# Optimization experiments

Measured on AMD Instinct MI355X. Metric: run time of the kernel, lower is better.

Reference implementation:

```python
import jax, jax.numpy as jnp
import numpy as np

BS, NQ, DIMS = 4, 6400, 256
NH, NL, NP, NQUEUE = 8, 1, 4, 2


def ms_deform_attn(value, shapes_np, starts_np, loc, attn):
    # value: [B, Nv, H, D]; loc: [B, Nq, H, L, P, 2] in [0,1]; attn: [B, Nq, H, L, P]
    B, Nv, H, D = value.shape
    _, Nq, _, L, P, _ = loc.shape
    out = jnp.zeros((B, H, Nq, D), loc.dtype)
    for l in range(L):
        Hl, Wl = int(shapes_np[l, 0]), int(shapes_np[l, 1])
        s = int(starts_np[l])
        vl = value[:, s:s + Hl * Wl].transpose(0, 2, 1, 3)  # [B,H,HW,D]
        # grid_sample align_corners=False pixel coords
        x = loc[:, :, :, l, :, 0] * Wl - 0.5  # [B,Nq,H,P]
        y = loc[:, :, :, l, :, 1] * Hl - 0.5
        x0 = jnp.floor(x); y0 = jnp.floor(y)
        dx = x - x0; dy = y - y0
        x0i = x0.astype(jnp.int32); y0i = y0.astype(jnp.int32)
        acc = jnp.zeros((B, H, Nq * P, D), loc.dtype)
        corners = [(x0i, y0i, (1 - dx) * (1 - dy)),
                   (x0i + 1, y0i, dx * (1 - dy)),
                   (x0i, y0i + 1, (1 - dx) * dy),
                   (x0i + 1, y0i + 1, dx * dy)]
        for xi, yi, w in corners:
            valid = (xi >= 0) & (xi < Wl) & (yi >= 0) & (yi < Hl)
            idx = jnp.clip(yi, 0, Hl - 1) * Wl + jnp.clip(xi, 0, Wl - 1)  # [B,Nq,H,P]
            idx_t = idx.transpose(0, 2, 1, 3).reshape(B, H, Nq * P, 1)
            g = jnp.take_along_axis(vl, idx_t, axis=2)  # [B,H,Nq*P,D]
            wv = jnp.where(valid, w, 0.0).transpose(0, 2, 1, 3).reshape(B, H, Nq * P, 1)
            acc = acc + g * wv
        acc = acc.reshape(B, H, Nq, P, D)
        wl = attn[:, :, :, l].transpose(0, 2, 1, 3)  # [B,H,Nq,P]
        out = out + jnp.einsum('bhnpd,bhnp->bhnd', acc, wl)
    return out.transpose(0, 2, 1, 3).reshape(B, Nq, H * D)


def setup_inputs() -> dict:
    key = jax.random.key(0)
    ks = jax.random.split(key, 12)
    d2 = DIMS * NQUEUE
    noff = NQUEUE * NH * NL * NP * 2
    nattn = NQUEUE * NH * NL * NP
    sc = 1.0 / np.sqrt(DIMS)
    return {
        'query': jax.random.normal(ks[0], (BS, NQ, DIMS), jnp.float32),
        'voxbev': jax.random.normal(ks[1], (BS, NQ, DIMS), jnp.float32),
        'reference_points': jax.random.uniform(ks[2], (BS * NQUEUE, NQ, NL, 2), jnp.float32),
        'spatial_shapes': jnp.array([[80, 80]], dtype=jnp.int64),
        'level_start_index': jnp.array([0], dtype=jnp.int64),
        'Wv': jax.random.normal(ks[3], (DIMS, DIMS), jnp.float32) * sc,
        'bv': jax.random.normal(ks[4], (DIMS,), jnp.float32) * 0.01,
        'Woff': jax.random.normal(ks[5], (d2, noff), jnp.float32) * (1.0 / np.sqrt(d2)),
        'boff': jax.random.normal(ks[6], (noff,), jnp.float32),
        'Wattn': jax.random.normal(ks[7], (d2, nattn), jnp.float32) * (1.0 / np.sqrt(d2)),
        'battn': jax.random.normal(ks[8], (nattn,), jnp.float32) * 0.01,
        'Wo': jax.random.normal(ks[9], (DIMS, DIMS), jnp.float32) * sc,
        'bo': jax.random.normal(ks[10], (DIMS,), jnp.float32) * 0.01,
    }


def reference(query, voxbev, reference_points, spatial_shapes, level_start_index,
              Wv, bv, Woff, boff, Wattn, battn, Wo, bo):
    bs, nq, dims = query.shape
    shapes_np = np.asarray(spatial_shapes)
    starts_np = np.asarray(level_start_index)
    identity = query
    # value = stack([query, voxbev], 1).reshape(bs*2, nq, dims) -> interleaved [q0,v0,q1,v1,...]
    value = jnp.stack([query, voxbev], 1).reshape(bs * NQUEUE, nq, dims)
    qcat = jnp.concatenate([value[:bs], query], -1)  # [bs, nq, 2*dims]
    v = (value @ Wv + bv).reshape(bs * NQUEUE, nq, NH, dims // NH)
    off = (qcat @ Woff + boff).reshape(bs, nq, NH, NQUEUE, NL, NP, 2)
    attn = (qcat @ Wattn + battn).reshape(bs, nq, NH, NQUEUE, NL * NP)
    attn = jax.nn.softmax(attn, axis=-1).reshape(bs, nq, NH, NQUEUE, NL, NP)
    attn = attn.transpose(0, 3, 1, 2, 4, 5).reshape(bs * NQUEUE, nq, NH, NL, NP)
    off = off.transpose(0, 3, 1, 2, 4, 5, 6).reshape(bs * NQUEUE, nq, NH, NL, NP, 2)
    # offset normalizer: (W, H) per level
    norm = jnp.stack([spatial_shapes[:, 1], spatial_shapes[:, 0]], -1).astype(off.dtype)  # [L,2]
    loc = reference_points[:, :, None, :, None, :] + off / norm[None, None, None, :, None, :]
    out = ms_deform_attn(v, shapes_np, starts_np, loc, attn)  # [bs*2, nq, dims]
    out = out.reshape(bs, NQUEUE, nq, dims).mean(1)  # mean over queue
    out = out @ Wo + bo
    return out + identity  # dropout is identity in eval
```

## Files before the change

### kernel.cpp

```cpp
#include <hip/hip_runtime.h>
#include <hip/hip_bf16.h>

#define BS   4
#define NQ   6400
#define DIMS 256
#define NH   8
#define NP   4
#define GW   80
#define GH   80

typedef __hip_bfloat16 bf16;
typedef unsigned short ushort;
typedef __attribute__((ext_vector_type(8))) short short8;
typedef __attribute__((ext_vector_type(4))) float floatx4;

union bfu { bf16 h; ushort s; };
__device__ __forceinline__ ushort f2bs(float x) { bfu u; u.h = __float2bfloat16(x); return u.s; }
__device__ __forceinline__ float bs2f(ushort s) { return __uint_as_float(((unsigned)s) << 16); }
__device__ __forceinline__ float ldin(const void* p, size_t i, int isf) {
    return isf ? ((const float*)p)[i] : bs2f(((const ushort*)p)[i]);
}

__global__ void detect_k(const ushort* __restrict__ q, int* flag) {
    __shared__ int s;
    if (threadIdx.x == 0) s = 0;
    __syncthreads();
    int bad = 0;
    for (int j = 0; j < 16; ++j) {
        ushort v = q[threadIdx.x * 16 + j];
        int e = (v >> 7) & 0xFF;
        if (e > 160) bad = 1;
    }
    if (bad) atomicOr(&s, 1);
    __syncthreads();
    if (threadIdx.x == 0) *flag = s;
}

__global__ void wprep_k(
    const void* __restrict__ Wv, const void* __restrict__ bv,
    const void* __restrict__ Woff, const void* __restrict__ boff,
    const void* __restrict__ Wattn, const void* __restrict__ battn,
    const void* __restrict__ Wo, const void* __restrict__ bo,
    const int* __restrict__ flagp,
    ushort* __restrict__ WvT, ushort* __restrict__ WoaT, ushort* __restrict__ WoT,
    float* __restrict__ biasv, float* __restrict__ biasoa, float* __restrict__ biaso)
{
    const int isf = *flagp;
    const int i = blockIdx.x * 256 + threadIdx.x;
    const int n1 = 256 * 256, n2 = n1 + 192 * 512, n3 = n2 + 256 * 256;
    const int n4 = n3 + 256, n5 = n4 + 192, n6 = n5 + 256;
    if (i < n1) {
        int n = i >> 8, k = i & 255;
        WvT[i] = f2bs(ldin(Wv, (size_t)k * 256 + n, isf));
    } else if (i < n2) {
        int j = i - n1, n = j >> 9, k = j & 511;
        float v = (n < 128) ? ldin(Woff, (size_t)k * 128 + n, isf)
                            : ldin(Wattn, (size_t)k * 64 + (n - 128), isf);
        WoaT[j] = f2bs(v);
    } else if (i < n3) {
        int j = i - n2, n = j >> 8, k = j & 255;
        WoT[j] = f2bs(ldin(Wo, (size_t)k * 256 + n, isf));
    } else if (i < n4) {
        biasv[i - n3] = ldin(bv, i - n3, isf);
    } else if (i < n5) {
        int j = i - n4;
        biasoa[j] = (j < 128) ? ldin(boff, j, isf) : ldin(battn, j - 128, isf);
    } else if (i < n6) {
        biaso[i - n5] = ldin(bo, i - n5, isf);
    }
}

__global__ __launch_bounds__(256) void cvt_k(
    const void* __restrict__ query, const void* __restrict__ voxbev,
    const int* __restrict__ flagp,
    uint4* __restrict__ qb, uint4* __restrict__ vbv)
{
    if (*flagp == 0) return;
    const int t = blockIdx.x * 256 + threadIdx.x;
    const int half = 819200;
    const void* src = (t < half) ? query : voxbev;
    uint4* dst = (t < half) ? qb : vbv;
    const int j = (t < half) ? t : t - half;
    const float4* s = (const float4*)src + (size_t)j * 2;
    float4 a = s[0], b = s[1];
    uint4 o;
    o.x = ((unsigned)f2bs(a.y) << 16) | f2bs(a.x);
    o.y = ((unsigned)f2bs(a.w) << 16) | f2bs(a.z);
    o.z = ((unsigned)f2bs(b.y) << 16) | f2bs(b.x);
    o.w = ((unsigned)f2bs(b.w) << 16) | f2bs(b.z);
    dst[j] = o;
}

enum { A_VAL = 0, A_QCAT = 1, A_PLAIN = 2 };
enum { O_BF16 = 0, O_FINAL = 1, O_VPERM = 2, O_OAPERM = 3 };

template <int AMODE, int OMODE, int KTOT, int NX, int MG>
__global__ __launch_bounds__(256) void pgemm_k(
    const ushort* __restrict__ Apl, const ushort* __restrict__ BT,
    const float* __restrict__ biasf, void* __restrict__ C,
    const void* __restrict__ query_raw, const void* __restrict__ voxbev_raw,
    const ushort* __restrict__ qb, const ushort* __restrict__ vbv,
    const int* __restrict__ flagp)
{
    constexpr int N = NX * 64;
    constexpr int NPH = KTOT / 256;
    constexpr int SROW = 264;
    constexpr int CST = 67;
    constexpr int SMEMB = (64 * SROW * 2 > 128 * CST * 4) ? 64 * SROW * 2
                                                          : 128 * CST * 4;
    __shared__ __align__(16) char smem[SMEMB];
    short* pan = (short*)smem;
    float* cbf = (float*)smem;

    const int F = blockIdx.x;
    const int xcd = F & 7, l = F >> 3;
    const int n = l % NX;
    const int mg = (l / NX) * 8 + xcd;
    if (mg >= MG) return;
    const int bm = mg * 256, bn = n * 64;

    const int isf = *flagp;
    const int tid = threadIdx.x;
    const int lane = tid & 63, wv = tid >> 6;
    const int wm = wv * 64;
    const int fr = lane & 15, fq = (lane >> 4) * 8;

    const ushort* qsrc = isf ? qb  : (const ushort*)query_raw;
    const ushort* vsrc = isf ? vbv : (const ushort*)voxbev_raw;
    const ushort* aph[NPH];
    if (AMODE == A_PLAIN) {
        aph[0] = Apl + (size_t)bm * DIMS;
    } else {
        const int b = bm / NQ, q0 = bm - (bm / NQ) * NQ;
        aph[0] = ((b & 1) ? vsrc : qsrc) + (size_t)((b >> 1) * NQ + q0) * DIMS;
        if (AMODE == A_QCAT) aph[1] = qsrc + (size_t)(b * NQ + q0) * DIMS;
    }

    floatx4 acc[4][4] = {};

    for (int ph = 0; ph < NPH; ++ph) {
        if (ph > 0) __syncthreads();
        #pragma unroll
        for (int i = 0; i < 8; ++i) {
            const int c = tid * 8 + i;
            const int row = c >> 5, j = (c & 31) * 8;
            *(uint4*)&pan[row * SROW + j] =
                *(const uint4*)&BT[(size_t)(bn + row) * KTOT + ph * 256 + j];
        }
        __syncthreads();

        const ushort* ab = aph[ph];
        #pragma unroll
        for (int k0 = 0; k0 < 256; k0 += 32) {
            short8 af[4], bf[4];
            #pragma unroll
            for (int mt = 0; mt < 4; ++mt)
                af[mt] = *(const short8*)&ab[(size_t)(wm + mt * 16 + fr) * DIMS + k0 + fq];
            #pragma unroll
            for (int nt = 0; nt < 4; ++nt)
                bf[nt] = *(const short8*)&pan[(nt * 16 + fr) * SROW + k0 + fq];
            #pragma unroll
            for (int mt = 0; mt < 4; ++mt)
                #pragma unroll
                for (int nt = 0; nt < 4; ++nt)
                    acc[mt][nt] = __builtin_amdgcn_mfma_f32_16x16x32_bf16(
                        af[mt], bf[nt], acc[mt][nt], 0, 0, 0);
        }
    }

    const int col = lane & 15, rq = (lane >> 4) * 4;
    const int lbase = wm & 127;
    #pragma unroll
    for (int half = 0; half < 2; ++half) {
        __syncthreads();
        if ((wv >> 1) == half) {
            #pragma unroll
            for (int mt = 0; mt < 4; ++mt)
                #pragma unroll
                for (int nt = 0; nt < 4; ++nt)
                    #pragma unroll
                    for (int r = 0; r < 4; ++r)
                        cbf[(lbase + mt * 16 + rq + r) * CST + nt * 16 + col] =
                            acc[mt][nt][r];
        }
        __syncthreads();

        if (OMODE == O_FINAL && isf) {
            const int r16 = tid >> 4, cc = tid & 15;
            #pragma unroll
            for (int it = 0; it < 8; ++it) {
                const int lr = it * 16 + r16;
                const size_t g = (size_t)(bm + half * 128 + lr);
                float4 x = *(const float4*)&cbf[lr * CST + cc * 4];
                const ushort* rs = qsrc + g * DIMS + bn + cc * 4;
                x.x += biasf[bn + cc * 4 + 0] + bs2f(rs[0]);
                x.y += biasf[bn + cc * 4 + 1] + bs2f(rs[1]);
                x.z += biasf[bn + cc * 4 + 2] + bs2f(rs[2]);
                x.w += biasf[bn + cc * 4 + 3] + bs2f(rs[3]);
                *(float4*)((float*)C + g * N + bn + cc * 4) = x;
            }
        } else {
            const int r8 = tid >> 3, c8 = tid & 7;
            #pragma unroll
            for (int it = 0; it < 4; ++it) {
                const int lr = it * 32 + r8;
                const size_t g = (size_t)(bm + half * 128 + lr);
                float4 x0 = *(const float4*)&cbf[lr * CST + c8 * 8];
                float4 x1 = *(const float4*)&cbf[lr * CST + c8 * 8 + 4];
                float xs[8] = { x0.x, x0.y, x0.z, x0.w, x1.x, x1.y, x1.z, x1.w };
                #pragma unroll
                for (int e = 0; e < 8; ++e) xs[e] += biasf[bn + c8 * 8 + e];
                if (OMODE == O_FINAL) {
                    const ushort* rs = qsrc + g * DIMS + bn + c8 * 8;
                    #pragma unroll
                    for (int e = 0; e < 8; ++e) xs[e] += bs2f(rs[e]);
                }
                uint4 o;
                o.x = ((unsigned)f2bs(xs[1]) << 16) | f2bs(xs[0]);
                o.y = ((unsigned)f2bs(xs[3]) << 16) | f2bs(xs[2]);
                o.z = ((unsigned)f2bs(xs[5]) << 16) | f2bs(xs[4]);
                o.w = ((unsigned)f2bs(xs[7]) << 16) | f2bs(xs[6]);
                ushort* dstp;
                if (OMODE == O_VPERM) {
                    const int cc = bn + c8 * 8;
                    const int s = (int)(g / NQ), qq = (int)(g % NQ);
                    dstp = (ushort*)C + ((size_t)(s * 8 + (cc >> 5)) * NQ + qq) * 32
                                      + (cc & 31);
                } else if (OMODE == O_OAPERM) {
                    const int cc = bn + c8 * 8;
                    const int bb = (int)(g / NQ), qq = (int)(g % NQ);
                    int hh, off;
                    if (cc < 128) { hh = cc >> 4; off = cc & 15; }
                    else          { hh = (cc - 128) >> 3; off = 16; }
                    dstp = (ushort*)C + ((size_t)(bb * 8 + hh) * NQ + qq) * 24 + off;
                } else {
                    dstp = (ushort*)C + g * N + bn + c8 * 8;
                }
                *(uint4*)dstp = o;
            }
        }
    }
}

__global__ __launch_bounds__(256) void sample_k(
    const ushort* __restrict__ v,
    const ushort* __restrict__ offp,
    const void* __restrict__ refpts,
    const int* __restrict__ flagp,
    ushort* __restrict__ sampled)
{
    const int isf = *flagp;
    __shared__ int   sidx[64][2][17];
    __shared__ float swt [64][2][17];
    const int tid = threadIdx.x;
    const int j = blockIdx.x;
    const int h = j & 7;
    const int k = j >> 3;
    const int b = k / 100;
    const int q0 = (k % 100) * 64;

    if (tid < 128) {
        const int lq = tid >> 1, queue = tid & 1;
        const int q = q0 + lq;
        const ushort* rec = offp + ((size_t)(b * 8 + h) * NQ + q) * 24;
        const ushort* al = rec + 16 + queue * 4;
        float l0 = bs2f(al[0]), l1 = bs2f(al[1]), l2 = bs2f(al[2]), l3 = bs2f(al[3]);
        float mx = fmaxf(fmaxf(l0, l1), fmaxf(l2, l3));
        float e0 = __expf(l0 - mx), e1 = __expf(l1 - mx);
        float e2 = __expf(l2 - mx), e3 = __expf(l3 - mx);
        float inv = 0.5f / (e0 + e1 + e2 + e3);
        const int bq = b * 2 + queue;
        const float rx = ldin(refpts, ((size_t)bq * NQ + q) * 2 + 0, isf);
        const float ry = ldin(refpts, ((size_t)bq * NQ + q) * 2 + 1, isf);
        const ushort* od = rec + queue * 8;
        float ww[4] = { e0 * inv, e1 * inv, e2 * inv, e3 * inv };
        #pragma unroll
        for (int p = 0; p < NP; ++p) {
            const float x = rx * (float)GW + bs2f(od[p * 2 + 0]) - 0.5f;
            const float y = ry * (float)GH + bs2f(od[p * 2 + 1]) - 0.5f;
            const float x0f = floorf(x), y0f = floorf(y);
            const float dx = x - x0f, dy = y - y0f;
            const int x0 = (int)x0f, y0 = (int)y0f;
            const float wp = ww[p];
            const float cw4[4] = { wp * (1.0f - dx) * (1.0f - dy),
                                   wp * dx * (1.0f - dy),
                                   wp * (1.0f - dx) * dy,
                                   wp * dx * dy };
            #pragma unroll
            for (int c = 0; c < 4; ++c) {
                const int xs = x0 + (c & 1), ys = y0 + (c >> 1);
                const bool ok = (unsigned)xs < (unsigned)GW && (unsigned)ys < (unsigned)GH;
                const int xi = min(max(xs, 0), GW - 1);
                const int yi = min(max(ys, 0), GH - 1);
                sidx[lq][queue][p * 4 + c] = yi * GW + xi;
                swt [lq][queue][p * 4 + c] = ok ? cw4[c] : 0.0f;
            }
        }
    }
    __syncthreads();

    const int lq = tid >> 2, d8 = tid & 3;
    const int q = q0 + lq;
    float a[8] = {};
    #pragma unroll
    for (int queue = 0; queue < 2; ++queue) {
        const ushort* vb = v + (((size_t)(b * 2 + queue) * 8 + h) * NQ) * 32 + d8 * 8;
        #pragma unroll
        for (int hf = 0; hf < 2; ++hf) {
            uint4 g[8];
            #pragma unroll
            for (int u = 0; u < 8; ++u) {
                const int ci = sidx[lq][queue][hf * 8 + u];
                g[u] = *(const uint4*)&vb[(size_t)ci * 32];
            }
            __builtin_amdgcn_sched_barrier(0);
            #pragma unroll
            for (int u = 0; u < 8; ++u) {
                const float cw = swt[lq][queue][hf * 8 + u];
                a[0] += cw * bs2f((ushort)g[u].x); a[1] += cw * bs2f((ushort)(g[u].x >> 16));
                a[2] += cw * bs2f((ushort)g[u].y); a[3] += cw * bs2f((ushort)(g[u].y >> 16));
                a[4] += cw * bs2f((ushort)g[u].z); a[5] += cw * bs2f((ushort)(g[u].z >> 16));
                a[6] += cw * bs2f((ushort)g[u].w); a[7] += cw * bs2f((ushort)(g[u].w >> 16));
            }
        }
    }
    uint4 o;
    o.x = ((unsigned)f2bs(a[1]) << 16) | f2bs(a[0]);
    o.y = ((unsigned)f2bs(a[3]) << 16) | f2bs(a[2]);
    o.z = ((unsigned)f2bs(a[5]) << 16) | f2bs(a[4]);
    o.w = ((unsigned)f2bs(a[7]) << 16) | f2bs(a[6]);
    *(uint4*)&sampled[((size_t)b * NQ + q) * DIMS + h * 32 + d8 * 8] = o;
}

extern "C" void kernel_launch(void* const* d_in, const int* in_sizes, int n_in,
                              void* d_out, int out_size, void* d_ws, size_t ws_size,
                              hipStream_t stream)
{
    const void* query  = d_in[0];
    const void* voxbev = d_in[1];
    const void* refpts = d_in[2];
    const void* Wv   = d_in[5];  const void* bv    = d_in[6];
    const void* Woff = d_in[7];  const void* boff  = d_in[8];
    const void* Wattn= d_in[9];  const void* battn = d_in[10];
    const void* Wo   = d_in[11]; const void* bo    = d_in[12];

    char* p = (char*)d_ws;
    int* flag = (int*)p;             p += 256;
    ushort* WvT  = (ushort*)p;       p += 256 * 256 * 2;
    ushort* WoaT = (ushort*)p;       p += 192 * 512 * 2;
    ushort* WoT  = (ushort*)p;       p += 256 * 256 * 2;
    float* biasv  = (float*)p;       p += 1024;
    float* biasoa = (float*)p;       p += 1024;
    float* biaso  = (float*)p;       p += 1024;
    ushort* qb   = (ushort*)p;       p += (size_t)BS * NQ * DIMS * 2;
    ushort* vbv  = (ushort*)p;       p += (size_t)BS * NQ * DIMS * 2;
    ushort* v_ws = (ushort*)p;       p += (size_t)2 * BS * NQ * DIMS * 2;
    ushort* offraw = (ushort*)p;     p += (size_t)BS * NQ * 192 * 2;
    ushort* sampled = (ushort*)p;

    detect_k<<<1, 256, 0, stream>>>((const ushort*)query, flag);
    wprep_k<<<899, 256, 0, stream>>>(Wv, bv, Woff, boff, Wattn, battn, Wo, bo,
                                     flag, WvT, WoaT, WoT, biasv, biasoa, biaso);
    cvt_k<<<6400, 256, 0, stream>>>(query, voxbev, flag, (uint4*)qb, (uint4*)vbv);

    pgemm_k<A_VAL, O_VPERM, 256, 4, 200><<<800, 256, 0, stream>>>(
        nullptr, WvT, biasv, (void*)v_ws, query, voxbev, qb, vbv, flag);

    pgemm_k<A_QCAT, O_OAPERM, 512, 3, 100><<<312, 256, 0, stream>>>(
        nullptr, WoaT, biasoa, (void*)offraw, query, voxbev, qb, vbv, flag);

    sample_k<<<3200, 256, 0, stream>>>(v_ws, offraw, refpts, flag, sampled);

    pgemm_k<A_PLAIN, O_FINAL, 256, 4, 100><<<416, 256, 0, stream>>>(
        sampled, WoT, biaso, d_out, query, voxbev, qb, vbv, flag);
}
```

Before: 217.6 us.

## Merge prep kernels, stage offsets in LDS, and software-pipeline sampling gathers

```diff
diff --git a/kernel.cpp b/kernel.cpp
--- a/kernel.cpp
+++ b/kernel.cpp
@@ -36,59 +36,58 @@
     if (threadIdx.x == 0) *flag = s;
 }
 
-__global__ void wprep_k(
+__global__ __launch_bounds__(256) void prep_k(
     const void* __restrict__ Wv, const void* __restrict__ bv,
     const void* __restrict__ Woff, const void* __restrict__ boff,
     const void* __restrict__ Wattn, const void* __restrict__ battn,
     const void* __restrict__ Wo, const void* __restrict__ bo,
     const int* __restrict__ flagp,
     ushort* __restrict__ WvT, ushort* __restrict__ WoaT, ushort* __restrict__ WoT,
-    float* __restrict__ biasv, float* __restrict__ biasoa, float* __restrict__ biaso)
+    float* __restrict__ biasv, float* __restrict__ biasoa, float* __restrict__ biaso,
+    const void* __restrict__ query, const void* __restrict__ voxbev,
+    uint4* __restrict__ qb, uint4* __restrict__ vbv)
 {
     const int isf = *flagp;
-    const int i = blockIdx.x * 256 + threadIdx.x;
-    const int n1 = 256 * 256, n2 = n1 + 192 * 512, n3 = n2 + 256 * 256;
-    const int n4 = n3 + 256, n5 = n4 + 192, n6 = n5 + 256;
-    if (i < n1) {
-        int n = i >> 8, k = i & 255;
-        WvT[i] = f2bs(ldin(Wv, (size_t)k * 256 + n, isf));
-    } else if (i < n2) {
-        int j = i - n1, n = j >> 9, k = j & 511;
-        float v = (n < 128) ? ldin(Woff, (size_t)k * 128 + n, isf)
-                            : ldin(Wattn, (size_t)k * 64 + (n - 128), isf);
-        WoaT[j] = f2bs(v);
-    } else if (i < n3) {
-        int j = i - n2, n = j >> 8, k = j & 255;
-        WoT[j] = f2bs(ldin(Wo, (size_t)k * 256 + n, isf));
-    } else if (i < n4) {
-        biasv[i - n3] = ldin(bv, i - n3, isf);
-    } else if (i < n5) {
-        int j = i - n4;
-        biasoa[j] = (j < 128) ? ldin(boff, j, isf) : ldin(battn, j - 128, isf);
-    } else if (i < n6) {
-        biaso[i - n5] = ldin(bo, i - n5, isf);
-    }
-}
-
-__global__ __launch_bounds__(256) void cvt_k(
-    const void* __restrict__ query, const void* __restrict__ voxbev,
-    const int* __restrict__ flagp,
-    uint4* __restrict__ qb, uint4* __restrict__ vbv)
-{
-    if (*flagp == 0) return;
-    const int t = blockIdx.x * 256 + threadIdx.x;
-    const int half = 819200;
-    const void* src = (t < half) ? query : voxbev;
-    uint4* dst = (t < half) ? qb : vbv;
-    const int j = (t < half) ? t : t - half;
-    const float4* s = (const float4*)src + (size_t)j * 2;
-    float4 a = s[0], b = s[1];
-    uint4 o;
-    o.x = ((unsigned)f2bs(a.y) << 16) | f2bs(a.x);
-    o.y = ((unsigned)f2bs(a.w) << 16) | f2bs(a.z);
-    o.z = ((unsigned)f2bs(b.y) << 16) | f2bs(b.x);
-    o.w = ((unsigned)f2bs(b.w) << 16) | f2bs(b.z);
-    dst[j] = o;
+    const int bid = blockIdx.x;
+    if (bid < 899) {
+        const int i = bid * 256 + threadIdx.x;
+        const int n1 = 256 * 256, n2 = n1 + 192 * 512, n3 = n2 + 256 * 256;
+        const int n4 = n3 + 256, n5 = n4 + 192, n6 = n5 + 256;
+        if (i < n1) {
+            int n = i >> 8, k = i & 255;
+            WvT[i] = f2bs(ldin(Wv, (size_t)k * 256 + n, isf));
+        } else if (i < n2) {
+            int j = i - n1, n = j >> 9, k = j & 511;
+            float v = (n < 128) ? ldin(Woff, (size_t)k * 128 + n, isf)
+                                : ldin(Wattn, (size_t)k * 64 + (n - 128), isf);
+            WoaT[j] = f2bs(v);
+        } else if (i < n3) {
+            int j = i - n2, n = j >> 8, k = j & 255;
+            WoT[j] = f2bs(ldin(Wo, (size_t)k * 256 + n, isf));
+        } else if (i < n4) {
+            biasv[i - n3] = ldin(bv, i - n3, isf);
+        } else if (i < n5) {
+            int j = i - n4;
+            biasoa[j] = (j < 128) ? ldin(boff, j, isf) : ldin(battn, j - 128, isf);
+        } else if (i < n6) {
+            biaso[i - n5] = ldin(bo, i - n5, isf);
+        }
+    } else {
+        if (isf == 0) return;
+        const int t = (bid - 899) * 256 + threadIdx.x;
+        const int half = 819200;
+        const void* src = (t < half) ? query : voxbev;
+        uint4* dst = (t < half) ? qb : vbv;
+        const int j = (t < half) ? t : t - half;
+        const float4* s = (const float4*)src + (size_t)j * 2;
+        float4 a = s[0], b = s[1];
+        uint4 o;
+        o.x = ((unsigned)f2bs(a.y) << 16) | f2bs(a.x);
+        o.y = ((unsigned)f2bs(a.w) << 16) | f2bs(a.z);
+        o.z = ((unsigned)f2bs(b.y) << 16) | f2bs(b.x);
+        o.w = ((unsigned)f2bs(b.w) << 16) | f2bs(b.z);
+        dst[j] = o;
+    }
 }
 
 enum { A_VAL = 0, A_QCAT = 1, A_PLAIN = 2 };
@@ -242,6 +241,13 @@
     }
 }
 
+__device__ __forceinline__ void fma8(float* a, const uint4& g, float cw) {
+    a[0] += cw * bs2f((ushort)g.x);  a[1] += cw * bs2f((ushort)(g.x >> 16));
+    a[2] += cw * bs2f((ushort)g.y);  a[3] += cw * bs2f((ushort)(g.y >> 16));
+    a[4] += cw * bs2f((ushort)g.z);  a[5] += cw * bs2f((ushort)(g.z >> 16));
+    a[6] += cw * bs2f((ushort)g.w);  a[7] += cw * bs2f((ushort)(g.w >> 16));
+}
+
 __global__ __launch_bounds__(256) void sample_k(
     const ushort* __restrict__ v,
     const ushort* __restrict__ offp,
@@ -252,6 +258,8 @@
     const int isf = *flagp;
     __shared__ int   sidx[64][2][17];
     __shared__ float swt [64][2][17];
+    __shared__ __align__(16) ushort srec[64 * 24];
+    __shared__ __align__(16) char   sref[1024];
     const int tid = threadIdx.x;
     const int j = blockIdx.x;
     const int h = j & 7;
@@ -259,19 +267,38 @@
     const int b = k / 100;
     const int q0 = (k % 100) * 64;
 
+    const ushort* recg = offp + ((size_t)(b * 8 + h) * NQ + q0) * 24;
+    if (tid < 192) ((uint4*)srec)[tid] = ((const uint4*)recg)[tid];
+    if (isf) {
+        if (tid >= 192) {
+            const int jj = tid - 192, qu = jj >> 5, ii = jj & 31;
+            const uint4* src = (const uint4*)((const float*)refpts
+                                + ((size_t)(b * 2 + qu) * NQ + q0) * 2);
+            ((uint4*)sref)[qu * 32 + ii] = src[ii];
+        }
+    } else {
+        if (tid >= 192 && tid < 224) {
+            const int jj = tid - 192, qu = jj >> 4, ii = jj & 15;
+            const uint4* src = (const uint4*)((const ushort*)refpts
+                                + ((size_t)(b * 2 + qu) * NQ + q0) * 2);
+            ((uint4*)sref)[qu * 16 + ii] = src[ii];
+        }
+    }
+    __syncthreads();
+
     if (tid < 128) {
         const int lq = tid >> 1, queue = tid & 1;
-        const int q = q0 + lq;
-        const ushort* rec = offp + ((size_t)(b * 8 + h) * NQ + q) * 24;
+        const ushort* rec = srec + lq * 24;
         const ushort* al = rec + 16 + queue * 4;
         float l0 = bs2f(al[0]), l1 = bs2f(al[1]), l2 = bs2f(al[2]), l3 = bs2f(al[3]);
         float mx = fmaxf(fmaxf(l0, l1), fmaxf(l2, l3));
         float e0 = __expf(l0 - mx), e1 = __expf(l1 - mx);
         float e2 = __expf(l2 - mx), e3 = __expf(l3 - mx);
         float inv = 0.5f / (e0 + e1 + e2 + e3);
-        const int bq = b * 2 + queue;
-        const float rx = ldin(refpts, ((size_t)bq * NQ + q) * 2 + 0, isf);
-        const float ry = ldin(refpts, ((size_t)bq * NQ + q) * 2 + 1, isf);
+        const float rx = isf ? ((const float*)sref)[(queue * 64 + lq) * 2 + 0]
+                             : bs2f(((const ushort*)sref)[(queue * 64 + lq) * 2 + 0]);
+        const float ry = isf ? ((const float*)sref)[(queue * 64 + lq) * 2 + 1]
+                             : bs2f(((const ushort*)sref)[(queue * 64 + lq) * 2 + 1]);
         const ushort* od = rec + queue * 8;
         float ww[4] = { e0 * inv, e1 * inv, e2 * inv, e3 * inv };
         #pragma unroll
@@ -301,29 +328,30 @@
 
     const int lq = tid >> 2, d8 = tid & 3;
     const int q = q0 + lq;
+    const ushort* vb0 = v + (((size_t)(b * 2 + 0) * 8 + h) * NQ) * 32 + d8 * 8;
+    const ushort* vb1 = vb0 + (size_t)8 * NQ * 32;
     float a[8] = {};
-    #pragma unroll
-    for (int queue = 0; queue < 2; ++queue) {
-        const ushort* vb = v + (((size_t)(b * 2 + queue) * 8 + h) * NQ) * 32 + d8 * 8;
-        #pragma unroll
-        for (int hf = 0; hf < 2; ++hf) {
-            uint4 g[8];
-            #pragma unroll
-            for (int u = 0; u < 8; ++u) {
-                const int ci = sidx[lq][queue][hf * 8 + u];
-                g[u] = *(const uint4*)&vb[(size_t)ci * 32];
-            }
-            __builtin_amdgcn_sched_barrier(0);
-            #pragma unroll
-            for (int u = 0; u < 8; ++u) {
-                const float cw = swt[lq][queue][hf * 8 + u];
-                a[0] += cw * bs2f((ushort)g[u].x); a[1] += cw * bs2f((ushort)(g[u].x >> 16));
-                a[2] += cw * bs2f((ushort)g[u].y); a[3] += cw * bs2f((ushort)(g[u].y >> 16));
-                a[4] += cw * bs2f((ushort)g[u].z); a[5] += cw * bs2f((ushort)(g[u].z >> 16));
-                a[6] += cw * bs2f((ushort)g[u].w); a[7] += cw * bs2f((ushort)(g[u].w >> 16));
-            }
-        }
-    }
+    uint4 g0[8], g1[8];
+    #pragma unroll
+    for (int u = 0; u < 8; ++u) g0[u] = *(const uint4*)&vb0[(size_t)sidx[lq][0][u] * 32];
+    #pragma unroll
+    for (int u = 0; u < 8; ++u) g1[u] = *(const uint4*)&vb0[(size_t)sidx[lq][0][8 + u] * 32];
+    __builtin_amdgcn_sched_barrier(0);
+    #pragma unroll
+    for (int u = 0; u < 8; ++u) fma8(a, g0[u], swt[lq][0][u]);
+    #pragma unroll
+    for (int u = 0; u < 8; ++u) g0[u] = *(const uint4*)&vb1[(size_t)sidx[lq][1][u] * 32];
+    __builtin_amdgcn_sched_barrier(0);
+    #pragma unroll
+    for (int u = 0; u < 8; ++u) fma8(a, g1[u], swt[lq][0][8 + u]);
+    #pragma unroll
+    for (int u = 0; u < 8; ++u) g1[u] = *(const uint4*)&vb1[(size_t)sidx[lq][1][8 + u] * 32];
+    __builtin_amdgcn_sched_barrier(0);
+    #pragma unroll
+    for (int u = 0; u < 8; ++u) fma8(a, g0[u], swt[lq][1][u]);
+    #pragma unroll
+    for (int u = 0; u < 8; ++u) fma8(a, g1[u], swt[lq][1][8 + u]);
+
     uint4 o;
     o.x = ((unsigned)f2bs(a[1]) << 16) | f2bs(a[0]);
     o.y = ((unsigned)f2bs(a[3]) << 16) | f2bs(a[2]);
@@ -359,9 +387,10 @@
     ushort* sampled = (ushort*)p;
 
     detect_k<<<1, 256, 0, stream>>>((const ushort*)query, flag);
-    wprep_k<<<899, 256, 0, stream>>>(Wv, bv, Woff, boff, Wattn, battn, Wo, bo,
-                                     flag, WvT, WoaT, WoT, biasv, biasoa, biaso);
-    cvt_k<<<6400, 256, 0, stream>>>(query, voxbev, flag, (uint4*)qb, (uint4*)vbv);
+
+    prep_k<<<7299, 256, 0, stream>>>(Wv, bv, Woff, boff, Wattn, battn, Wo, bo,
+                                     flag, WvT, WoaT, WoT, biasv, biasoa, biaso,
+                                     query, voxbev, (uint4*)qb, (uint4*)vbv);
 
     pgemm_k<A_VAL, O_VPERM, 256, 4, 200><<<800, 256, 0, stream>>>(
         nullptr, WvT, biasv, (void*)v_ws, query, voxbev, qb, vbv, flag);
```

After: 216.7 us. Within noise of the previous version (-0.4%).

## Merge detect/prep/convert kernels and fuse the two input GEMMs into one launch

Applied to the files above, without the earlier changes.

```diff
diff --git a/kernel.cpp b/kernel.cpp
--- a/kernel.cpp
+++ b/kernel.cpp
@@ -21,105 +21,102 @@
     return isf ? ((const float*)p)[i] : bs2f(((const ushort*)p)[i]);
 }
 
-__global__ void detect_k(const ushort* __restrict__ q, int* flag) {
-    __shared__ int s;
-    if (threadIdx.x == 0) s = 0;
-    __syncthreads();
+__device__ __forceinline__ int self_detect(const ushort* __restrict__ q, int tid) {
     int bad = 0;
-    for (int j = 0; j < 16; ++j) {
-        ushort v = q[threadIdx.x * 16 + j];
-        int e = (v >> 7) & 0xFF;
-        if (e > 160) bad = 1;
-    }
-    if (bad) atomicOr(&s, 1);
-    __syncthreads();
-    if (threadIdx.x == 0) *flag = s;
-}
-
-__global__ void wprep_k(
+    const uint4 u0 = ((const uint4*)q)[tid * 2];
+    const uint4 u1 = ((const uint4*)q)[tid * 2 + 1];
+    const unsigned w[8] = { u0.x, u0.y, u0.z, u0.w, u1.x, u1.y, u1.z, u1.w };
+    #pragma unroll
+    for (int j = 0; j < 8; ++j) {
+        if (((w[j] >> 7)  & 0xFF) > 160) bad = 1;
+        if (((w[j] >> 23) & 0xFF) > 160) bad = 1;
+    }
+    return __any(bad) ? 1 : 0;
+}
+
+__global__ __launch_bounds__(256) void prep_k(
     const void* __restrict__ Wv, const void* __restrict__ bv,
     const void* __restrict__ Woff, const void* __restrict__ boff,
     const void* __restrict__ Wattn, const void* __restrict__ battn,
     const void* __restrict__ Wo, const void* __restrict__ bo,
-    const int* __restrict__ flagp,
+    int* __restrict__ flagp,
     ushort* __restrict__ WvT, ushort* __restrict__ WoaT, ushort* __restrict__ WoT,
-    float* __restrict__ biasv, float* __restrict__ biasoa, float* __restrict__ biaso)
-{
-    const int isf = *flagp;
-    const int i = blockIdx.x * 256 + threadIdx.x;
-    const int n1 = 256 * 256, n2 = n1 + 192 * 512, n3 = n2 + 256 * 256;
-    const int n4 = n3 + 256, n5 = n4 + 192, n6 = n5 + 256;
-    if (i < n1) {
-        int n = i >> 8, k = i & 255;
-        WvT[i] = f2bs(ldin(Wv, (size_t)k * 256 + n, isf));
-    } else if (i < n2) {
-        int j = i - n1, n = j >> 9, k = j & 511;
-        float v = (n < 128) ? ldin(Woff, (size_t)k * 128 + n, isf)
-                            : ldin(Wattn, (size_t)k * 64 + (n - 128), isf);
-        WoaT[j] = f2bs(v);
-    } else if (i < n3) {
-        int j = i - n2, n = j >> 8, k = j & 255;
-        WoT[j] = f2bs(ldin(Wo, (size_t)k * 256 + n, isf));
-    } else if (i < n4) {
-        biasv[i - n3] = ldin(bv, i - n3, isf);
-    } else if (i < n5) {
-        int j = i - n4;
-        biasoa[j] = (j < 128) ? ldin(boff, j, isf) : ldin(battn, j - 128, isf);
-    } else if (i < n6) {
-        biaso[i - n5] = ldin(bo, i - n5, isf);
-    }
-}
-
-__global__ __launch_bounds__(256) void cvt_k(
+    float* __restrict__ biasv, float* __restrict__ biasoa, float* __restrict__ biaso,
     const void* __restrict__ query, const void* __restrict__ voxbev,
-    const int* __restrict__ flagp,
     uint4* __restrict__ qb, uint4* __restrict__ vbv)
 {
-    if (*flagp == 0) return;
-    const int t = blockIdx.x * 256 + threadIdx.x;
-    const int half = 819200;
-    const void* src = (t < half) ? query : voxbev;
-    uint4* dst = (t < half) ? qb : vbv;
-    const int j = (t < half) ? t : t - half;
-    const float4* s = (const float4*)src + (size_t)j * 2;
-    float4 a = s[0], b = s[1];
-    uint4 o;
-    o.x = ((unsigned)f2bs(a.y) << 16) | f2bs(a.x);
-    o.y = ((unsigned)f2bs(a.w) << 16) | f2bs(a.z);
-    o.z = ((unsigned)f2bs(b.y) << 16) | f2bs(b.x);
-    o.w = ((unsigned)f2bs(b.w) << 16) | f2bs(b.z);
-    dst[j] = o;
+    const int tid = threadIdx.x;
+    const int isf = self_detect((const ushort*)query, tid);
+    const int bid = blockIdx.x;
+    if (bid == 0 && tid == 0) *flagp = isf;
+    if (bid < 899) {
+        const int i = bid * 256 + tid;
+        const int n1 = 256 * 256, n2 = n1 + 192 * 512, n3 = n2 + 256 * 256;
+        const int n4 = n3 + 256, n5 = n4 + 192, n6 = n5 + 256;
+        if (i < n1) {
+            int n = i >> 8, k = i & 255;
+            WvT[i] = f2bs(ldin(Wv, (size_t)k * 256 + n, isf));
+        } else if (i < n2) {
+            int j = i - n1, n = j >> 9, k = j & 511;
+            float v = (n < 128) ? ldin(Woff, (size_t)k * 128 + n, isf)
+                                : ldin(Wattn, (size_t)k * 64 + (n - 128), isf);
+            WoaT[j] = f2bs(v);
+        } else if (i < n3) {
+            int j = i - n2, n = j >> 8, k = j & 255;
+            WoT[j] = f2bs(ldin(Wo, (size_t)k * 256 + n, isf));
+        } else if (i < n4) {
+            biasv[i - n3] = ldin(bv, i - n3, isf);
+        } else if (i < n5) {
+            int j = i - n4;
+            biasoa[j] = (j < 128) ? ldin(boff, j, isf) : ldin(battn, j - 128, isf);
+        } else if (i < n6) {
+            biaso[i - n5] = ldin(bo, i - n5, isf);
+        }
+    } else {
+        if (isf == 0) return;
+        const int t = (bid - 899) * 256 + tid;
+        const int half = 819200;
+        const void* src = (t < half) ? query : voxbev;
+        uint4* dst = (t < half) ? qb : vbv;
+        const int j = (t < half) ? t : t - half;
+        const float4* s = (const float4*)src + (size_t)j * 2;
+        float4 a = s[0], b = s[1];
+        uint4 o;
+        o.x = ((unsigned)f2bs(a.y) << 16) | f2bs(a.x);
+        o.y = ((unsigned)f2bs(a.w) << 16) | f2bs(a.z);
+        o.z = ((unsigned)f2bs(b.y) << 16) | f2bs(b.x);
+        o.w = ((unsigned)f2bs(b.w) << 16) | f2bs(b.z);
+        dst[j] = o;
+    }
 }
 
 enum { A_VAL = 0, A_QCAT = 1, A_PLAIN = 2 };
 enum { O_BF16 = 0, O_FINAL = 1, O_VPERM = 2, O_OAPERM = 3 };
 
+#define SROW 264
+#define CST  67
+#define SMEMB (128 * CST * 4)
+
 template <int AMODE, int OMODE, int KTOT, int NX, int MG>
-__global__ __launch_bounds__(256) void pgemm_k(
+__device__ __forceinline__ void pgemm_body(
+    const int F, char* smem,
     const ushort* __restrict__ Apl, const ushort* __restrict__ BT,
     const float* __restrict__ biasf, void* __restrict__ C,
     const void* __restrict__ query_raw, const void* __restrict__ voxbev_raw,
     const ushort* __restrict__ qb, const ushort* __restrict__ vbv,
-    const int* __restrict__ flagp)
+    const int isf)
 {
     constexpr int N = NX * 64;
     constexpr int NPH = KTOT / 256;
-    constexpr int SROW = 264;
-    constexpr int CST = 67;
-    constexpr int SMEMB = (64 * SROW * 2 > 128 * CST * 4) ? 64 * SROW * 2
-                                                          : 128 * CST * 4;
-    __shared__ __align__(16) char smem[SMEMB];
     short* pan = (short*)smem;
     float* cbf = (float*)smem;
 
-    const int F = blockIdx.x;
     const int xcd = F & 7, l = F >> 3;
     const int n = l % NX;
     const int mg = (l / NX) * 8 + xcd;
     if (mg >= MG) return;
     const int bm = mg * 256, bn = n * 64;
 
-    const int isf = *flagp;
     const int tid = threadIdx.x;
     const int lane = tid & 63, wv = tid >> 6;
     const int wm = wv * 64;
@@ -242,6 +239,40 @@
     }
 }
 
+__global__ __launch_bounds__(256) void gemm12_k(
+    const ushort* __restrict__ WvT, const float* __restrict__ biasv,
+    ushort* __restrict__ v_ws,
+    const ushort* __restrict__ WoaT, const float* __restrict__ biasoa,
+    ushort* __restrict__ offraw,
+    const void* __restrict__ query_raw, const void* __restrict__ voxbev_raw,
+    const ushort* __restrict__ qb, const ushort* __restrict__ vbv,
+    const int* __restrict__ flagp)
+{
+    __shared__ __align__(16) char smem[SMEMB];
+    const int isf = *flagp;
+    const int bid = blockIdx.x;
+    if (bid < 800) {
+        pgemm_body<A_VAL, O_VPERM, 256, 4, 200>(bid, smem,
+            nullptr, WvT, biasv, (void*)v_ws, query_raw, voxbev_raw, qb, vbv, isf);
+    } else {
+        pgemm_body<A_QCAT, O_OAPERM, 512, 3, 100>(bid - 800, smem,
+            nullptr, WoaT, biasoa, (void*)offraw, query_raw, voxbev_raw, qb, vbv, isf);
+    }
+}
+
+__global__ __launch_bounds__(256) void gemm4_k(
+    const ushort* __restrict__ Apl, const ushort* __restrict__ BT,
+    const float* __restrict__ biasf, void* __restrict__ C,
+    const void* __restrict__ query_raw, const void* __restrict__ voxbev_raw,
+    const ushort* __restrict__ qb, const ushort* __restrict__ vbv,
+    const int* __restrict__ flagp)
+{
+    __shared__ __align__(16) char smem[SMEMB];
+    const int isf = *flagp;
+    pgemm_body<A_PLAIN, O_FINAL, 256, 4, 100>(blockIdx.x, smem,
+        Apl, BT, biasf, C, query_raw, voxbev_raw, qb, vbv, isf);
+}
+
 __global__ __launch_bounds__(256) void sample_k(
     const ushort* __restrict__ v,
     const ushort* __restrict__ offp,
@@ -358,19 +389,15 @@
     ushort* offraw = (ushort*)p;     p += (size_t)BS * NQ * 192 * 2;
     ushort* sampled = (ushort*)p;
 
-    detect_k<<<1, 256, 0, stream>>>((const ushort*)query, flag);
-    wprep_k<<<899, 256, 0, stream>>>(Wv, bv, Woff, boff, Wattn, battn, Wo, bo,
-                                     flag, WvT, WoaT, WoT, biasv, biasoa, biaso);
-    cvt_k<<<6400, 256, 0, stream>>>(query, voxbev, flag, (uint4*)qb, (uint4*)vbv);
-
-    pgemm_k<A_VAL, O_VPERM, 256, 4, 200><<<800, 256, 0, stream>>>(
-        nullptr, WvT, biasv, (void*)v_ws, query, voxbev, qb, vbv, flag);
-
-    pgemm_k<A_QCAT, O_OAPERM, 512, 3, 100><<<312, 256, 0, stream>>>(
-        nullptr, WoaT, biasoa, (void*)offraw, query, voxbev, qb, vbv, flag);
+    prep_k<<<7299, 256, 0, stream>>>(Wv, bv, Woff, boff, Wattn, battn, Wo, bo,
+                                     flag, WvT, WoaT, WoT, biasv, biasoa, biaso,
+                                     query, voxbev, (uint4*)qb, (uint4*)vbv);
+
+    gemm12_k<<<1112, 256, 0, stream>>>(WvT, biasv, v_ws, WoaT, biasoa, offraw,
+                                       query, voxbev, qb, vbv, flag);
 
     sample_k<<<3200, 256, 0, stream>>>(v_ws, offraw, refpts, flag, sampled);
 
-    pgemm_k<A_PLAIN, O_FINAL, 256, 4, 100><<<416, 256, 0, stream>>>(
-        sampled, WoT, biaso, d_out, query, voxbev, qb, vbv, flag);
-}
+    gemm4_k<<<416, 256, 0, stream>>>(sampled, WoT, biaso, d_out,
+                                     query, voxbev, qb, vbv, flag);
+}
```

Result: faster. 203.5 us (-6.5%).
